# Optimization experiments

Hardware: AMD Instinct MI355X
Metric: run time of the kernel (lower is better)

The kernel has to match this reference:

```python
import jax, jax.numpy as jnp
import numpy as np

T = 128        # number of time points
D = 64         # flattened state dim (bs * z_dim, bs = 1)
H = 256        # hidden width of f-network
HK = 128       # hidden width of kernel network
MAX_IT = 3     # fixed-point iterations (args.max_iterations)


def setup_inputs() -> dict:
    key = jax.random.key(0)
    ks = jax.random.split(key, 6)
    g = lambda k, sh, sc: (jax.random.normal(k, sh, jnp.float32) * sc)
    z0 = jax.random.normal(ks[0], (1, D), jnp.float32)
    t = jnp.linspace(0.0, 1.0, T, dtype=jnp.float32)
    # f: D -> H -> D MLP (the 'func' integrand network)
    W1 = g(ks[1], (D, H), 1.0 / np.sqrt(D)); b1 = jnp.zeros((H,), jnp.float32)
    W2 = g(ks[2], (H, D), 1.0 / np.sqrt(H)); b2 = jnp.zeros((D,), jnp.float32)
    # kernel: (x, s) -> D*D matrix entries (the neural kernel K)
    Wk1 = g(ks[3], (2, HK), 1.0 / np.sqrt(2.0)); bk1 = jnp.zeros((HK,), jnp.float32)
    Wk2 = g(ks[4], (HK, D * D), 1.0 / np.sqrt(HK)); bk2 = jnp.zeros((D * D,), jnp.float32)
    return dict(z0=z0, t=t, W1=W1, b1=b1, W2=W2, b2=b2,
                Wk1=Wk1, bk1=bk1, Wk2=Wk2, bk2=bk2)


def _trapezoid_weights(t):
    """w[i, j]: trapezoid quadrature weight of node j for integral over [t0, t_i]."""
    dt = t[1] - t[0]  # uniform grid
    idx = jnp.arange(T)
    mask = (idx[None, :] <= idx[:, None]).astype(t.dtype)
    w = dt * mask
    w = w.at[(idx, idx)].multiply(0.5)   # halve right endpoint of each row
    w = w.at[:, 0].multiply(0.5)         # halve left endpoint
    w = w.at[0].set(0.0)                 # zero-length integral at t0
    return w


def _solve(z0, t, W1, b1, W2, b2, Wk1, bk1, Wk2, bk2):
    y0 = z0.reshape(-1)                                   # [D], solver flattens batch
    w = _trapezoid_weights(t)                             # [T, T]
    # Neural kernel K(x_i, s_j) -> [D, D], precomputed once on the grid.
    pairs = jnp.stack([jnp.broadcast_to(t[:, None], (T, T)),
                       jnp.broadcast_to(t[None, :], (T, T))], axis=-1)  # [T, T, 2]
    hK = jnp.tanh(pairs @ Wk1 + bk1)                      # [T, T, HK]
    K = (hK @ Wk2 + bk2).reshape(T, T, D, D)              # [T, T, D, D]

    def f(y):  # integrand network, applied over all time points
        return jnp.tanh(y @ W1 + b1) @ W2 + b2            # [T, D]

    def step(y, _):
        # G_i = \int_0^{x_i} K(x_i, s) f(y(s)) ds  (trapezoid on grid)
        G = jnp.einsum('ij,ijde,je->id', w, K, f(y))      # [T, D]
        # y'(x) = G(x)  =>  y_i = y0 + \int_0^{x_i} G(s) ds
        y_new = y0[None, :] + w @ G                       # [T, D]
        return y_new, None

    y_init = jnp.tile(y0[None, :], (T, 1))                # fixed-point initial guess
    y, _ = jax.lax.scan(step, y_init, None, length=MAX_IT)
    return y


def reference(z0, t, W1, b1, W2, b2, Wk1, bk1, Wk2, bk2):
    y = _solve(z0, t, W1, b1, W2, b2, Wk1, bk1, Wk2, bk2)  # [T, D]
    return y[-1].reshape(1, D)  # z[-1]: final state, shape [bs, dim]
```

## Files before the change

kernel.cpp:

```cpp
#include <hip/hip_runtime.h>
#include <hip/hip_bf16.h>

#define TT 128
#define DD 64
#define HH 256
#define HK 128
#define JH (TT*HK)
#define HD (HK*DD)
#define NCHUNK 64

__global__ void __launch_bounds__(256)
k_F0M0(const float* __restrict__ z0,
       const float* __restrict__ W1, const float* __restrict__ b1,
       const float* __restrict__ W2, const float* __restrict__ b2,
       const float* __restrict__ bk2, const float* __restrict__ Wk2,
       float* __restrict__ M0, float* __restrict__ bF0) {
    int bx = blockIdx.x, tid = threadIdx.x;
    int part = tid >> 6, d = tid & 63;
    __shared__ float red[4][64];
    __shared__ float ys[DD];
    __shared__ float hs[HH];
    __shared__ __attribute__((aligned(16))) float fs[DD];
    if (tid < DD) ys[tid] = z0[tid];
    __syncthreads();
    float acc = b1[tid];
    #pragma unroll 8
    for (int e = 0; e < DD; ++e) acc += ys[e] * W1[e * HH + tid];
    hs[tid] = tanhf(acc);
    __syncthreads();
    {
        float s = 0.f;
        #pragma unroll 8
        for (int h = part * 64; h < part * 64 + 64; ++h) s += hs[h] * W2[h * DD + d];
        red[part][d] = s;
    }
    __syncthreads();
    if (part == 0)
        fs[d] = b2[d] + red[0][d] + red[1][d] + red[2][d] + red[3][d];
    __syncthreads();
    if (bx == 0) {
        float s = 0.f;
        #pragma unroll
        for (int e = part * 16; e < part * 16 + 16; ++e) s += bk2[d * DD + e] * fs[e];
        red[part][d] = s;
        __syncthreads();
        if (part == 0)
            bF0[d] = red[0][d] + red[1][d] + red[2][d] + red[3][d];
    }
    int hd = bx * 256 + tid;
    const float* Wrow = Wk2 + (size_t)(hd >> 6) * (DD * DD) + (size_t)(hd & 63) * DD;
    float a = 0.f;
    #pragma unroll
    for (int e = 0; e < DD; e += 8) {
        float4 wa = *(const float4*)(Wrow + e);
        float4 wb = *(const float4*)(Wrow + e + 4);
        float4 fa = *(const float4*)&fs[e];
        float4 fb = *(const float4*)&fs[e + 4];
        a += fa.x*wa.x + fa.y*wa.y + fa.z*wa.z + fa.w*wa.w
           + fb.x*wb.x + fb.y*wb.y + fb.z*wb.z + fb.w*wb.w;
    }
    M0[hd] = a;
}

__global__ void __launch_bounds__(256)
k_G0(const float* __restrict__ t, const float* __restrict__ Wk1,
     const float* __restrict__ bk1, const float* __restrict__ M0,
     const float* __restrict__ bF0, float* __restrict__ G) {
    int i = blockIdx.x, tid = threadIdx.x;
    int part = tid >> 6, d = tid & 63;
    __shared__ float Bpart[2][HK];
    __shared__ float Bs[HK];
    __shared__ float red[4][64];
    float dt = t[1] - t[0];
    int h = tid & 127, half = tid >> 7;
    float b = 0.f;
    if (i > 0) {
        float wk0 = Wk1[h], wk1v = Wk1[HK + h], bk = bk1[h];
        float ti = t[i];
        for (int j = half; j <= i; j += 2) {
            float w = dt * ((j == 0 || j == i) ? 0.5f : 1.0f);
            b += w * tanhf(ti * wk0 + t[j] * wk1v + bk);
        }
    }
    Bpart[half][h] = b;
    __syncthreads();
    if (tid < HK) Bs[tid] = Bpart[0][tid] + Bpart[1][tid];
    __syncthreads();
    float a = 0.f;
    #pragma unroll 8
    for (int h2 = part * 32; h2 < part * 32 + 32; ++h2)
        a += Bs[h2] * M0[h2 * DD + d];
    red[part][d] = a;
    __syncthreads();
    if (part == 0) {
        float g = red[0][d] + red[1][d] + red[2][d] + red[3][d];
        if (i > 0) g += dt * (float)i * bF0[d];
        G[i * DD + d] = g;
    }
}

__global__ void __launch_bounds__(256)
k_F(const float* __restrict__ G, const float* __restrict__ z0,
    const float* __restrict__ t,
    const float* __restrict__ W1, const float* __restrict__ b1,
    const float* __restrict__ W2, const float* __restrict__ b2,
    const float* __restrict__ bk2,
    float* __restrict__ F, float* __restrict__ bF) {
    int j = blockIdx.x, tid = threadIdx.x;
    int part = tid >> 6, d = tid & 63;
    __shared__ float red[4][64];
    __shared__ float ys[DD];
    __shared__ float hs[HH];
    __shared__ float fs[DD];
    float dt = t[1] - t[0];
    {
        float s = 0.f;
        if (j > 0) {
            for (int jp = part; jp <= j; jp += 4) {
                float w = (jp == 0 || jp == j) ? 0.5f : 1.0f;
                s += w * G[jp * DD + d];
            }
        }
        red[part][d] = s;
        __syncthreads();
        if (part == 0)
            ys[d] = z0[d] + dt * (red[0][d] + red[1][d] + red[2][d] + red[3][d]);
    }
    __syncthreads();
    float acc = b1[tid];
    #pragma unroll 8
    for (int e = 0; e < DD; ++e) acc += ys[e] * W1[e * HH + tid];
    hs[tid] = tanhf(acc);
    __syncthreads();
    {
        float s = 0.f;
        #pragma unroll 8
        for (int h = part * 64; h < part * 64 + 64; ++h) s += hs[h] * W2[h * DD + d];
        red[part][d] = s;
    }
    __syncthreads();
    if (part == 0) {
        float a = b2[d] + red[0][d] + red[1][d] + red[2][d] + red[3][d];
        fs[d] = a;
        F[j * DD + d] = a;
    }
    __syncthreads();
    {
        float s = 0.f;
        #pragma unroll
        for (int e = part * 16; e < part * 16 + 16; ++e) s += bk2[d * DD + e] * fs[e];
        red[part][d] = s;
    }
    __syncthreads();
    if (part == 0)
        bF[j * DD + d] = red[0][d] + red[1][d] + red[2][d] + red[3][d];
}

__global__ void __launch_bounds__(256)
k_M(const float* __restrict__ F, const float* __restrict__ Wk2,
    float* __restrict__ M) {
    int tid = threadIdx.x;
    int hd = blockIdx.x * 256 + tid;
    int j0 = blockIdx.y * 8;
    __shared__ __attribute__((aligned(16))) float Fs[8][64];
    for (int k = tid; k < 8 * DD; k += 256) Fs[k >> 6][k & 63] = F[j0 * DD + k];
    __syncthreads();
    float acc[8] = {0.f,0.f,0.f,0.f,0.f,0.f,0.f,0.f};
    const float* Wrow = Wk2 + (size_t)(hd >> 6) * (DD * DD) + (size_t)(hd & 63) * DD;
    for (int e = 0; e < DD; e += 8) {
        float4 wa = *(const float4*)(Wrow + e);
        float4 wb = *(const float4*)(Wrow + e + 4);
        #pragma unroll
        for (int r = 0; r < 8; ++r) {
            float4 f0 = *(const float4*)&Fs[r][e];
            float4 f1 = *(const float4*)&Fs[r][e + 4];
            acc[r] += f0.x*wa.x + f0.y*wa.y + f0.z*wa.z + f0.w*wa.w
                    + f1.x*wb.x + f1.y*wb.y + f1.z*wb.z + f1.w*wb.w;
        }
    }
    #pragma unroll
    for (int r = 0; r < 8; ++r) M[(size_t)(j0 + r) * HD + hd] = acc[r];
}

__global__ void __launch_bounds__(256)
k_G1(const float* __restrict__ t, const float* __restrict__ Wk1,
     const float* __restrict__ bk1, const float* __restrict__ M,
     float* __restrict__ P, const float* __restrict__ z0,
     float* __restrict__ out, int final_it) {
    int itile = blockIdx.x, c = blockIdx.y;
    if (c > 4 * itile + 3) return;
    __shared__ __attribute__((aligned(16))) float As[8 * 256];
    __shared__ float red[4][8][64];
    int tid = threadIdx.x, sub = tid >> 6, d = tid & 63;

    {
        float dt = t[1] - t[0];
        int h = tid & 127;
        int j = 2 * c + (tid >> 7);
        float wk0 = Wk1[h], wk1v = Wk1[HK + h], bk = bk1[h];
        float tj = t[j];
        #pragma unroll
        for (int k = 0; k < 8; ++k) {
            int i = itile * 8 + k;
            float w = (i == 0 || j > i) ? 0.f : dt * ((j == 0 || j == i) ? 0.5f : 1.0f);
            As[k * 256 + tid] = w * tanhf(t[i] * wk0 + tj * wk1v + bk);
        }
    }
    if (final_it && itile == 0 && c == 0 && tid < DD) out[tid] = z0[tid];
    __syncthreads();

    float acc[8] = {0.f,0.f,0.f,0.f,0.f,0.f,0.f,0.f};
    const float* Mp = M + ((size_t)c * 256) * DD + d;
    int jl0 = sub * 64;
    for (int jl = jl0; jl < jl0 + 64; jl += 8) {
        float m0 = Mp[(size_t)(jl + 0) * DD];
        float m1 = Mp[(size_t)(jl + 1) * DD];
        float m2 = Mp[(size_t)(jl + 2) * DD];
        float m3 = Mp[(size_t)(jl + 3) * DD];
        float m4 = Mp[(size_t)(jl + 4) * DD];
        float m5 = Mp[(size_t)(jl + 5) * DD];
        float m6 = Mp[(size_t)(jl + 6) * DD];
        float m7 = Mp[(size_t)(jl + 7) * DD];
        #pragma unroll
        for (int r = 0; r < 8; ++r) {
            float4 a0 = *(const float4*)&As[r * 256 + jl];
            float4 a1 = *(const float4*)&As[r * 256 + jl + 4];
            acc[r] += a0.x*m0 + a0.y*m1 + a0.z*m2 + a0.w*m3
                    + a1.x*m4 + a1.y*m5 + a1.z*m6 + a1.w*m7;
        }
    }
    #pragma unroll
    for (int r = 0; r < 8; ++r) red[sub][r][d] = acc[r];
    __syncthreads();
    if (sub == 0) {
        #pragma unroll
        for (int r = 0; r < 8; ++r) {
            float v = red[0][r][d] + red[1][r][d] + red[2][r][d] + red[3][r][d];
            P[(size_t)c * (TT * DD) + (itile * 8 + r) * DD + d] = v;
        }
    }
}

__global__ void __launch_bounds__(256)
k_Gfin(const float* __restrict__ P, const float* __restrict__ bF,
       const float* __restrict__ t, float* __restrict__ G,
       float* __restrict__ out, int final_it) {
    int j = blockIdx.x, tid = threadIdx.x;
    int part = tid >> 6, d = tid & 63;
    __shared__ float red[4][64];
    float dt = t[1] - t[0];
    float a = 0.f;
    int cmax = j >> 1;
    for (int c = part; c <= cmax; c += 4) a += P[(size_t)c * (TT * DD) + j * DD + d];
    if (j > 0) {
        float s = 0.f;
        for (int jp = part; jp <= j; jp += 4) {
            float w = (jp == 0 || jp == j) ? 0.5f : 1.0f;
            s += w * bF[jp * DD + d];
        }
        a += dt * s;
    }
    red[part][d] = a;
    __syncthreads();
    if (part == 0) {
        float v = red[0][d] + red[1][d] + red[2][d] + red[3][d];
        G[j * DD + d] = v;
        if (final_it) {
            float wj = (j == 0 || j == TT - 1) ? 0.5f : 1.0f;
            atomicAdd(&out[d], dt * wj * v);
        }
    }
}

extern "C" void kernel_launch(void* const* d_in, const int* in_sizes, int n_in,
                              void* d_out, int out_size, void* d_ws, size_t ws_size,
                              hipStream_t stream) {
    const float* z0  = (const float*)d_in[0];
    const float* t   = (const float*)d_in[1];
    const float* W1  = (const float*)d_in[2];
    const float* b1  = (const float*)d_in[3];
    const float* W2  = (const float*)d_in[4];
    const float* b2  = (const float*)d_in[5];
    const float* Wk1 = (const float*)d_in[6];
    const float* bk1 = (const float*)d_in[7];
    const float* Wk2 = (const float*)d_in[8];
    const float* bk2 = (const float*)d_in[9];
    float* out = (float*)d_out;

    float* ws  = (float*)d_ws;
    float* M   = ws;
    float* F   = M   + (size_t)TT*HK*DD;
    float* bF  = F   + TT*DD;
    float* G   = bF  + TT*DD;
    float* P   = G   + TT*DD;
    float* M0  = P   + (size_t)NCHUNK*TT*DD;
    float* bF0 = M0  + HD;

    k_F0M0<<<32, 256, 0, stream>>>(z0, W1, b1, W2, b2, bk2, Wk2, M0, bF0);
    k_G0<<<TT, 256, 0, stream>>>(t, Wk1, bk1, M0, bF0, G);
    for (int it = 1; it < 3; ++it) {
        int fin = (it == 2) ? 1 : 0;
        k_F<<<TT, 256, 0, stream>>>(G, z0, t, W1, b1, W2, b2, bk2, F, bF);
        k_M<<<dim3(32, 16), 256, 0, stream>>>(F, Wk2, M);
        k_G1<<<dim3(16, NCHUNK), 256, 0, stream>>>(t, Wk1, bk1, M, P, z0, out, fin);
        k_Gfin<<<TT, 256, 0, stream>>>(P, bF, t, G, out, fin);
    }
}
```

Before: 185.7 us.

## Restructure solver into fused F/M kernel, precomputed A table, atomic G accumulation

Restructures the pipeline. The tanh kernel-weight table A is computed once in an init kernel, and the init also folds the M0 and G0 stages together. The f-network evaluation is fused with the M = F·Wk2 product, four blocks per time point, with the f-MLP recomputed redundantly in each of the four. The partial-sum buffer P and the k_Gfin reduction are replaced by atomicAdd into G, with the bF trapezoid terms also added there. A single output kernel computes the final trapezoid. The launch count drops from 10 to 6, at the cost of redundant MLP work, atomics, and a 2M-float A buffer that is read back from memory.

New measurement: 347.1 us. 86.9% more time.

```diff
diff --git a/kernel.cpp b/kernel.cpp
--- a/kernel.cpp
+++ b/kernel.cpp
@@ -1,26 +1,56 @@
 #include <hip/hip_runtime.h>
-#include <hip/hip_bf16.h>
 
 #define TT 128
 #define DD 64
 #define HH 256
-#define HK 128
-#define JH (TT*HK)
-#define HD (HK*DD)
-#define NCHUNK 64
+#define HKD 128
+#define HD (HKD*DD)
 
 __global__ void __launch_bounds__(256)
-k_F0M0(const float* __restrict__ z0,
+k_init(const float* __restrict__ z0, const float* __restrict__ t,
        const float* __restrict__ W1, const float* __restrict__ b1,
        const float* __restrict__ W2, const float* __restrict__ b2,
-       const float* __restrict__ bk2, const float* __restrict__ Wk2,
-       float* __restrict__ M0, float* __restrict__ bF0) {
-    int bx = blockIdx.x, tid = threadIdx.x;
-    int part = tid >> 6, d = tid & 63;
+       const float* __restrict__ Wk1, const float* __restrict__ bk1,
+       const float* __restrict__ Wk2, const float* __restrict__ bk2,
+       float* __restrict__ A, float* __restrict__ G0)
+{
+    const int b = blockIdx.x, tid = threadIdx.x;
+    const float dt = t[1] - t[0];
+
+    if (b >= 128) {
+        const int ab = b - 128;
+        const int h = tid & 127;
+        const float wk0 = Wk1[h], wk1v = Wk1[HKD + h], bk = bk1[h];
+        const int i = ab >> 2;
+        const float ti = t[i];
+        const int base = ab * 4096;
+        #pragma unroll 4
+        for (int k = 0; k < 16; ++k) {
+            int n = base + k * 256 + tid;
+            int j = (n >> 7) & 127;
+            float w = (i == 0 || j > i) ? 0.f : dt * ((j == 0 || j == i) ? 0.5f : 1.f);
+            float v = 0.f;
+            if (w != 0.f)
+                v = w * tanhf(ti * wk0 + t[j] * wk1v + bk);
+            A[n] = v;
+        }
+        return;
+    }
+
+    const int i = b;
+    const int part = tid >> 6, d = tid & 63;
     __shared__ float red[4][64];
     __shared__ float ys[DD];
     __shared__ float hs[HH];
     __shared__ __attribute__((aligned(16))) float fs[DD];
+    __shared__ float Bpart[2][HKD];
+    __shared__ float Bs[HKD];
+
+    if (i == 0) {
+        if (part == 0) G0[d] = 0.f;
+        return;
+    }
+
     if (tid < DD) ys[tid] = z0[tid];
     __syncthreads();
     float acc = b1[tid];
@@ -38,87 +68,79 @@
     if (part == 0)
         fs[d] = b2[d] + red[0][d] + red[1][d] + red[2][d] + red[3][d];
     __syncthreads();
-    if (bx == 0) {
-        float s = 0.f;
-        #pragma unroll
-        for (int e = part * 16; e < part * 16 + 16; ++e) s += bk2[d * DD + e] * fs[e];
-        red[part][d] = s;
-        __syncthreads();
-        if (part == 0)
-            bF0[d] = red[0][d] + red[1][d] + red[2][d] + red[3][d];
-    }
-    int hd = bx * 256 + tid;
-    const float* Wrow = Wk2 + (size_t)(hd >> 6) * (DD * DD) + (size_t)(hd & 63) * DD;
-    float a = 0.f;
-    #pragma unroll
-    for (int e = 0; e < DD; e += 8) {
-        float4 wa = *(const float4*)(Wrow + e);
-        float4 wb = *(const float4*)(Wrow + e + 4);
-        float4 fa = *(const float4*)&fs[e];
-        float4 fb = *(const float4*)&fs[e + 4];
-        a += fa.x*wa.x + fa.y*wa.y + fa.z*wa.z + fa.w*wa.w
-           + fb.x*wb.x + fb.y*wb.y + fb.z*wb.z + fb.w*wb.w;
-    }
-    M0[hd] = a;
-}
-
-__global__ void __launch_bounds__(256)
-k_G0(const float* __restrict__ t, const float* __restrict__ Wk1,
-     const float* __restrict__ bk1, const float* __restrict__ M0,
-     const float* __restrict__ bF0, float* __restrict__ G) {
-    int i = blockIdx.x, tid = threadIdx.x;
-    int part = tid >> 6, d = tid & 63;
-    __shared__ float Bpart[2][HK];
-    __shared__ float Bs[HK];
-    __shared__ float red[4][64];
-    float dt = t[1] - t[0];
-    int h = tid & 127, half = tid >> 7;
-    float b = 0.f;
-    if (i > 0) {
-        float wk0 = Wk1[h], wk1v = Wk1[HK + h], bk = bk1[h];
-        float ti = t[i];
+
+    {
+        const int h = tid & 127, half = tid >> 7;
+        const float wk0 = Wk1[h], wk1v = Wk1[HKD + h], bk = bk1[h];
+        const float ti = t[i];
+        float bsum = 0.f;
         for (int j = half; j <= i; j += 2) {
             float w = dt * ((j == 0 || j == i) ? 0.5f : 1.0f);
-            b += w * tanhf(ti * wk0 + t[j] * wk1v + bk);
-        }
-    }
-    Bpart[half][h] = b;
-    __syncthreads();
-    if (tid < HK) Bs[tid] = Bpart[0][tid] + Bpart[1][tid];
-    __syncthreads();
+            bsum += w * tanhf(ti * wk0 + t[j] * wk1v + bk);
+        }
+        Bpart[half][h] = bsum;
+    }
+    __syncthreads();
+    if (tid < HKD) Bs[tid] = Bpart[0][tid] + Bpart[1][tid];
+    __syncthreads();
+
     float a = 0.f;
-    #pragma unroll 8
-    for (int h2 = part * 32; h2 < part * 32 + 32; ++h2)
-        a += Bs[h2] * M0[h2 * DD + d];
+    for (int h2 = part * 32; h2 < part * 32 + 32; ++h2) {
+        const float* Wrow = Wk2 + (size_t)h2 * 4096 + (size_t)d * DD;
+        float m = 0.f;
+        #pragma unroll
+        for (int e = 0; e < DD; e += 8) {
+            float4 wa = *(const float4*)(Wrow + e);
+            float4 wb = *(const float4*)(Wrow + e + 4);
+            float4 fa = *(const float4*)&fs[e];
+            float4 fb = *(const float4*)&fs[e + 4];
+            m += fa.x*wa.x + fa.y*wa.y + fa.z*wa.z + fa.w*wa.w
+               + fb.x*wb.x + fb.y*wb.y + fb.z*wb.z + fb.w*wb.w;
+        }
+        a += Bs[h2] * m;
+    }
     red[part][d] = a;
     __syncthreads();
     if (part == 0) {
+        const float* br = bk2 + (size_t)d * DD;
+        float bf = 0.f;
+        #pragma unroll
+        for (int e = 0; e < DD; e += 8) {
+            float4 wa = *(const float4*)(br + e);
+            float4 wb = *(const float4*)(br + e + 4);
+            float4 fa = *(const float4*)&fs[e];
+            float4 fb = *(const float4*)&fs[e + 4];
+            bf += fa.x*wa.x + fa.y*wa.y + fa.z*wa.z + fa.w*wa.w
+                + fb.x*wb.x + fb.y*wb.y + fb.z*wb.z + fb.w*wb.w;
+        }
         float g = red[0][d] + red[1][d] + red[2][d] + red[3][d];
-        if (i > 0) g += dt * (float)i * bF0[d];
-        G[i * DD + d] = g;
+        G0[i * DD + d] = g + dt * (float)i * bf;
     }
 }
 
 __global__ void __launch_bounds__(256)
-k_F(const float* __restrict__ G, const float* __restrict__ z0,
-    const float* __restrict__ t,
-    const float* __restrict__ W1, const float* __restrict__ b1,
-    const float* __restrict__ W2, const float* __restrict__ b2,
-    const float* __restrict__ bk2,
-    float* __restrict__ F, float* __restrict__ bF) {
-    int j = blockIdx.x, tid = threadIdx.x;
-    int part = tid >> 6, d = tid & 63;
+k_FM(const float* __restrict__ Gin, float* __restrict__ Gz,
+     const float* __restrict__ z0, const float* __restrict__ t,
+     const float* __restrict__ W1, const float* __restrict__ b1,
+     const float* __restrict__ W2, const float* __restrict__ b2,
+     const float* __restrict__ bk2, const float* __restrict__ Wk2,
+     float* __restrict__ M, float* __restrict__ bF)
+{
+    const int b = blockIdx.x, tid = threadIdx.x;
+    const int j = b >> 2, q = b & 3;
+    const int part = tid >> 6, d = tid & 63;
     __shared__ float red[4][64];
     __shared__ float ys[DD];
     __shared__ float hs[HH];
-    __shared__ float fs[DD];
-    float dt = t[1] - t[0];
+    __shared__ __attribute__((aligned(16))) float fs[DD];
+    const float dt = t[1] - t[0];
+
     {
         float s = 0.f;
         if (j > 0) {
             for (int jp = part; jp <= j; jp += 4) {
                 float w = (jp == 0 || jp == j) ? 0.5f : 1.0f;
-                s += w * G[jp * DD + d];
+                s += w * Gin[jp * DD + d];
             }
         }
         red[part][d] = s;
@@ -127,6 +149,7 @@
             ys[d] = z0[d] + dt * (red[0][d] + red[1][d] + red[2][d] + red[3][d]);
     }
     __syncthreads();
+
     float acc = b1[tid];
     #pragma unroll 8
     for (int e = 0; e < DD; ++e) acc += ys[e] * W1[e * HH + tid];
@@ -139,79 +162,63 @@
         red[part][d] = s;
     }
     __syncthreads();
-    if (part == 0) {
-        float a = b2[d] + red[0][d] + red[1][d] + red[2][d] + red[3][d];
-        fs[d] = a;
-        F[j * DD + d] = a;
-    }
-    __syncthreads();
-    {
+    if (part == 0)
+        fs[d] = b2[d] + red[0][d] + red[1][d] + red[2][d] + red[3][d];
+    __syncthreads();
+
+    if (q == 0) {
         float s = 0.f;
         #pragma unroll
         for (int e = part * 16; e < part * 16 + 16; ++e) s += bk2[d * DD + e] * fs[e];
         red[part][d] = s;
-    }
-    __syncthreads();
-    if (part == 0)
-        bF[j * DD + d] = red[0][d] + red[1][d] + red[2][d] + red[3][d];
+        __syncthreads();
+        if (part == 0) {
+            bF[j * DD + d] = red[0][d] + red[1][d] + red[2][d] + red[3][d];
+            Gz[j * DD + d] = 0.f;
+        }
+    }
+
+    const int hb = q * 2048;
+    #pragma unroll
+    for (int k = 0; k < 8; ++k) {
+        int hd = hb + k * 256 + tid;
+        const float* Wrow = Wk2 + (size_t)hd * DD;
+        float a = 0.f;
+        #pragma unroll
+        for (int e = 0; e < DD; e += 8) {
+            float4 wa = *(const float4*)(Wrow + e);
+            float4 wb = *(const float4*)(Wrow + e + 4);
+            float4 fa = *(const float4*)&fs[e];
+            float4 fb = *(const float4*)&fs[e + 4];
+            a += fa.x*wa.x + fa.y*wa.y + fa.z*wa.z + fa.w*wa.w
+               + fb.x*wb.x + fb.y*wb.y + fb.z*wb.z + fb.w*wb.w;
+        }
+        M[(size_t)j * HD + hd] = a;
+    }
 }
 
 __global__ void __launch_bounds__(256)
-k_M(const float* __restrict__ F, const float* __restrict__ Wk2,
-    float* __restrict__ M) {
-    int tid = threadIdx.x;
-    int hd = blockIdx.x * 256 + tid;
-    int j0 = blockIdx.y * 8;
-    __shared__ __attribute__((aligned(16))) float Fs[8][64];
-    for (int k = tid; k < 8 * DD; k += 256) Fs[k >> 6][k & 63] = F[j0 * DD + k];
-    __syncthreads();
-    float acc[8] = {0.f,0.f,0.f,0.f,0.f,0.f,0.f,0.f};
-    const float* Wrow = Wk2 + (size_t)(hd >> 6) * (DD * DD) + (size_t)(hd & 63) * DD;
-    for (int e = 0; e < DD; e += 8) {
-        float4 wa = *(const float4*)(Wrow + e);
-        float4 wb = *(const float4*)(Wrow + e + 4);
-        #pragma unroll
-        for (int r = 0; r < 8; ++r) {
-            float4 f0 = *(const float4*)&Fs[r][e];
-            float4 f1 = *(const float4*)&Fs[r][e + 4];
-            acc[r] += f0.x*wa.x + f0.y*wa.y + f0.z*wa.z + f0.w*wa.w
-                    + f1.x*wb.x + f1.y*wb.y + f1.z*wb.z + f1.w*wb.w;
-        }
-    }
-    #pragma unroll
-    for (int r = 0; r < 8; ++r) M[(size_t)(j0 + r) * HD + hd] = acc[r];
-}
-
-__global__ void __launch_bounds__(256)
-k_G1(const float* __restrict__ t, const float* __restrict__ Wk1,
-     const float* __restrict__ bk1, const float* __restrict__ M,
-     float* __restrict__ P, const float* __restrict__ z0,
-     float* __restrict__ out, int final_it) {
-    int itile = blockIdx.x, c = blockIdx.y;
+k_G1a(const float* __restrict__ A, const float* __restrict__ M,
+      const float* __restrict__ bF, const float* __restrict__ t,
+      float* __restrict__ Gout)
+{
+    const int itile = blockIdx.x, c = blockIdx.y;
     if (c > 4 * itile + 3) return;
     __shared__ __attribute__((aligned(16))) float As[8 * 256];
     __shared__ float red[4][8][64];
-    int tid = threadIdx.x, sub = tid >> 6, d = tid & 63;
-
-    {
-        float dt = t[1] - t[0];
-        int h = tid & 127;
-        int j = 2 * c + (tid >> 7);
-        float wk0 = Wk1[h], wk1v = Wk1[HK + h], bk = bk1[h];
-        float tj = t[j];
-        #pragma unroll
-        for (int k = 0; k < 8; ++k) {
-            int i = itile * 8 + k;
-            float w = (i == 0 || j > i) ? 0.f : dt * ((j == 0 || j == i) ? 0.5f : 1.0f);
-            As[k * 256 + tid] = w * tanhf(t[i] * wk0 + tj * wk1v + bk);
-        }
-    }
-    if (final_it && itile == 0 && c == 0 && tid < DD) out[tid] = z0[tid];
+    const int tid = threadIdx.x, part = tid >> 6, d = tid & 63;
+    const float dt = t[1] - t[0];
+
+    const float* Asrc = A + ((size_t)(itile * 8) * TT + 2 * c) * HKD;
+    for (int qq = tid; qq < 8 * 64; qq += 256) {
+        int r = qq >> 6, c4 = qq & 63;
+        ((float4*)As)[r * 64 + c4] = *(const float4*)(Asrc + (size_t)r * TT * HKD + c4 * 4);
+    }
     __syncthreads();
 
     float acc[8] = {0.f,0.f,0.f,0.f,0.f,0.f,0.f,0.f};
     const float* Mp = M + ((size_t)c * 256) * DD + d;
-    int jl0 = sub * 64;
+    const int jl0 = part * 64;
     for (int jl = jl0; jl < jl0 + 64; jl += 8) {
         float m0 = Mp[(size_t)(jl + 0) * DD];
         float m1 = Mp[(size_t)(jl + 1) * DD];
@@ -230,46 +237,45 @@
         }
     }
     #pragma unroll
-    for (int r = 0; r < 8; ++r) red[sub][r][d] = acc[r];
-    __syncthreads();
-    if (sub == 0) {
+    for (int r = 0; r < 8; ++r) red[part][r][d] = acc[r];
+    __syncthreads();
+    if (part == 0) {
         #pragma unroll
         for (int r = 0; r < 8; ++r) {
             float v = red[0][r][d] + red[1][r][d] + red[2][r][d] + red[3][r][d];
-            P[(size_t)c * (TT * DD) + (itile * 8 + r) * DD + d] = v;
+            atomicAdd(&Gout[(itile * 8 + r) * DD + d], v);
+        }
+        if (c == 0) {
+            const int i0 = itile * 8;
+            float run = 0.5f * bF[d];
+            int p = 0;
+            for (int r = 0; r < 8; ++r) {
+                int i = i0 + r;
+                if (i == 0) continue;
+                while (p < i - 1) { ++p; run += bF[p * DD + d]; }
+                float term = dt * (run + 0.5f * bF[i * DD + d]);
+                atomicAdd(&Gout[i * DD + d], term);
+            }
         }
     }
 }
 
 __global__ void __launch_bounds__(256)
-k_Gfin(const float* __restrict__ P, const float* __restrict__ bF,
-       const float* __restrict__ t, float* __restrict__ G,
-       float* __restrict__ out, int final_it) {
-    int j = blockIdx.x, tid = threadIdx.x;
-    int part = tid >> 6, d = tid & 63;
+k_out(const float* __restrict__ G, const float* __restrict__ z0,
+      const float* __restrict__ t, float* __restrict__ out)
+{
+    const int tid = threadIdx.x, part = tid >> 6, d = tid & 63;
     __shared__ float red[4][64];
-    float dt = t[1] - t[0];
-    float a = 0.f;
-    int cmax = j >> 1;
-    for (int c = part; c <= cmax; c += 4) a += P[(size_t)c * (TT * DD) + j * DD + d];
-    if (j > 0) {
-        float s = 0.f;
-        for (int jp = part; jp <= j; jp += 4) {
-            float w = (jp == 0 || jp == j) ? 0.5f : 1.0f;
-            s += w * bF[jp * DD + d];
-        }
-        a += dt * s;
-    }
-    red[part][d] = a;
-    __syncthreads();
-    if (part == 0) {
-        float v = red[0][d] + red[1][d] + red[2][d] + red[3][d];
-        G[j * DD + d] = v;
-        if (final_it) {
-            float wj = (j == 0 || j == TT - 1) ? 0.5f : 1.0f;
-            atomicAdd(&out[d], dt * wj * v);
-        }
-    }
+    const float dt = t[1] - t[0];
+    float s = 0.f;
+    for (int j = part; j < TT; j += 4) {
+        float w = (j == 0 || j == TT - 1) ? 0.5f : 1.0f;
+        s += w * G[j * DD + d];
+    }
+    red[part][d] = s;
+    __syncthreads();
+    if (part == 0)
+        out[d] = z0[d] + dt * (red[0][d] + red[1][d] + red[2][d] + red[3][d]);
 }
 
 extern "C" void kernel_launch(void* const* d_in, const int* in_sizes, int n_in,
@@ -287,22 +293,17 @@
     const float* bk2 = (const float*)d_in[9];
     float* out = (float*)d_out;
 
-    float* ws  = (float*)d_ws;
-    float* M   = ws;
-    float* F   = M   + (size_t)TT*HK*DD;
-    float* bF  = F   + TT*DD;
-    float* G   = bF  + TT*DD;
-    float* P   = G   + TT*DD;
-    float* M0  = P   + (size_t)NCHUNK*TT*DD;
-    float* bF0 = M0  + HD;
-
-    k_F0M0<<<32, 256, 0, stream>>>(z0, W1, b1, W2, b2, bk2, Wk2, M0, bF0);
-    k_G0<<<TT, 256, 0, stream>>>(t, Wk1, bk1, M0, bF0, G);
-    for (int it = 1; it < 3; ++it) {
-        int fin = (it == 2) ? 1 : 0;
-        k_F<<<TT, 256, 0, stream>>>(G, z0, t, W1, b1, W2, b2, bk2, F, bF);
-        k_M<<<dim3(32, 16), 256, 0, stream>>>(F, Wk2, M);
-        k_G1<<<dim3(16, NCHUNK), 256, 0, stream>>>(t, Wk1, bk1, M, P, z0, out, fin);
-        k_Gfin<<<TT, 256, 0, stream>>>(P, bF, t, G, out, fin);
-    }
-}
+    float* ws = (float*)d_ws;
+    float* A  = ws;
+    float* M  = A  + (size_t)TT*TT*HKD;
+    float* Ga = M  + (size_t)TT*HKD*DD;
+    float* Gb = Ga + TT*DD;
+    float* bF = Gb + TT*DD;
+
+    k_init<<<640, 256, 0, stream>>>(z0, t, W1, b1, W2, b2, Wk1, bk1, Wk2, bk2, A, Ga);
+    k_FM<<<512, 256, 0, stream>>>(Ga, Gb, z0, t, W1, b1, W2, b2, bk2, Wk2, M, bF);
+    k_G1a<<<dim3(16, 64), 256, 0, stream>>>(A, M, bF, t, Gb);
+    k_FM<<<512, 256, 0, stream>>>(Gb, Ga, z0, t, W1, b1, W2, b2, bk2, Wk2, M, bF);
+    k_G1a<<<dim3(16, 64), 256, 0, stream>>>(A, M, bF, t, Ga);
+    k_out<<<1, 256, 0, stream>>>(Ga, z0, t, out);
+}
```
